# Optimization experiments

Hardware: AMD Instinct MI355X
Metric: run time of the kernel (lower is better)

Reference implementation:

```python
import jax, jax.numpy as jnp
import numpy as np

N_NODES = 100000
N_EDGES = 800000
IN_CH = 64
NUM_CLASSES = 64


def setup_inputs() -> dict:
    key = jax.random.key(0)
    k_x, k_e, k_w, k_b, k_fw, k_fb = jax.random.split(key, 6)
    x = jax.random.normal(k_x, (N_NODES, IN_CH), dtype=jnp.float32)
    edge_index = jax.random.randint(k_e, (2, N_EDGES), 0, N_NODES, dtype=jnp.int64)
    # GCNConv(in_channels, in_channels): weight + bias
    s = 1.0 / np.sqrt(IN_CH)
    W = jax.random.uniform(k_w, (IN_CH, IN_CH), jnp.float32, -s, s)
    b = jax.random.uniform(k_b, (IN_CH,), jnp.float32, -s, s)
    # LayerNorm(in_channels)
    gamma = jnp.ones((IN_CH,), jnp.float32)
    beta = jnp.zeros((IN_CH,), jnp.float32)
    # fc: Linear(in_channels, num_classes)
    fcW = jax.random.uniform(k_fw, (IN_CH, NUM_CLASSES), jnp.float32, -s, s)
    fcb = jax.random.uniform(k_fb, (NUM_CLASSES,), jnp.float32, -s, s)
    return {"x": x, "edge_index": edge_index, "W": W, "b": b,
            "gamma": gamma, "beta": beta, "fcW": fcW, "fcb": fcb}


def _gcn_conv(x, src, dst, W, b, n_nodes):
    # PyG GCNConv: linear transform, add self-loops, sym-normalized scatter-add.
    loop = jnp.arange(n_nodes, dtype=src.dtype)
    src = jnp.concatenate([src, loop])
    dst = jnp.concatenate([dst, loop])
    deg = jax.ops.segment_sum(jnp.ones(dst.shape, x.dtype), dst, num_segments=n_nodes)
    dinv = jax.lax.rsqrt(deg)  # deg >= 1 thanks to self-loops
    norm = dinv[src] * dinv[dst]  # [E+N]
    h = x @ W  # [N, C]
    msg = h[src] * norm[:, None]  # [E+N, C]
    out = jax.ops.segment_sum(msg, dst, num_segments=n_nodes)
    return out + b


def _layer_norm(x, gamma, beta, eps=1e-5):
    mu = jnp.mean(x, axis=-1, keepdims=True)
    var = jnp.mean(jnp.square(x - mu), axis=-1, keepdims=True)
    return (x - mu) * jax.lax.rsqrt(var + eps) * gamma + beta


def reference(x, edge_index, W, b, gamma, beta, fcW, fcb):
    n_nodes = x.shape[0]
    src, dst = edge_index[0], edge_index[1]
    h = _gcn_conv(x, src, dst, W, b, n_nodes)
    h = _layer_norm(h, gamma, beta)
    h = jax.nn.relu(h)
    # dropout is identity in eval mode
    h = h * x  # dot-product gating with original input
    return h @ fcW + fcb
```

## Files before the change

### kernel.cpp

```cpp
#include <hip/hip_runtime.h>
#include <hip/hip_fp16.h>
#include <math.h>

#define N_NODES 100000
#define N_EDGES 800000
#define C 64
#define SLOT 48
#define XW_BLOCKS 391
#define EDGE_BLOCKS 3125

#define XCOMP(v, c) ((c) == 0 ? (v).x : (c) == 1 ? (v).y : (c) == 2 ? (v).z : (v).w)

__device__ inline unsigned pk2h(float a, float b) {
    __half2 h = __floats2half2_rn(a, b);
    return *(unsigned*)&h;
}

__global__ __launch_bounds__(256) void fill_xw_kernel(
        const int* __restrict__ src, const int* __restrict__ dst,
        int* __restrict__ cnt, int* __restrict__ srcs,
        const float* __restrict__ x, const float* __restrict__ W,
        uint4* __restrict__ hs4) {
    if (blockIdx.x >= XW_BLOCKS) {
        const int e = (blockIdx.x - XW_BLOCKS) * 256 + threadIdx.x;
        const int d = dst[e];
        const int p = atomicAdd(&cnt[d], 1);
        if (p < SLOT) srcs[d * SLOT + p] = src[e];
        return;
    }
    const int lane = threadIdx.x & 63;
    const int wv = blockIdx.x * 4 + (threadIdx.x >> 6);
    const int r = wv * 64 + lane;
    const bool valid = r < N_NODES;
    const float4* __restrict__ x4 = (const float4*)x;

    float acc[C];
#pragma unroll
    for (int m = 0; m < C; ++m) acc[m] = 0.0f;

    for (int kk = 0; kk < 4; ++kk) {
        float4 xv[4];
#pragma unroll
        for (int q = 0; q < 4; ++q)
            xv[q] = valid ? x4[r * 16 + kk * 4 + q] : make_float4(0.f, 0.f, 0.f, 0.f);
#pragma unroll
        for (int j = 0; j < 16; ++j) {
            const float xs = XCOMP(xv[j >> 2], j & 3);
            const float* __restrict__ wr = W + (kk * 16 + j) * C;
#pragma unroll
            for (int m = 0; m < C; ++m) acc[m] = fmaf(xs, wr[m], acc[m]);
        }
    }

    if (valid) {
#pragma unroll
        for (int q = 0; q < 8; ++q) {
            uint4 u;
            u.x = pk2h(acc[8 * q + 0], acc[8 * q + 1]);
            u.y = pk2h(acc[8 * q + 2], acc[8 * q + 3]);
            u.z = pk2h(acc[8 * q + 4], acc[8 * q + 5]);
            u.w = pk2h(acc[8 * q + 6], acc[8 * q + 7]);
            hs4[r * 8 + q] = u;
        }
    }
}

__global__ __launch_bounds__(256) void gather_ln_kernel(
        const uint4* __restrict__ hs4, const int* __restrict__ cnt,
        const int* __restrict__ srcs, const float4* __restrict__ x4,
        const float* __restrict__ b, const float* __restrict__ gamma,
        const float* __restrict__ beta, float4* __restrict__ g4) {
    const int lane = threadIdx.x & 63;
    const int n = blockIdx.x * 4 + (threadIdx.x >> 6);
    const int eg = lane >> 3;
    const int cg = lane & 7;

    const int deg = cnt[n];
    const int dg = deg < SLOT ? deg : SLOT;
    const int base = n * SLOT;
    const float dinv = rsqrtf((float)deg + 1.0f);

    float a[8];
    if (eg == 0) {
        const uint4 hv = hs4[n * 8 + cg];
        const float2 f0 = __half22float2(*(const __half2*)&hv.x);
        const float2 f1 = __half22float2(*(const __half2*)&hv.y);
        const float2 f2 = __half22float2(*(const __half2*)&hv.z);
        const float2 f3 = __half22float2(*(const __half2*)&hv.w);
        a[0] = dinv * f0.x; a[1] = dinv * f0.y; a[2] = dinv * f1.x; a[3] = dinv * f1.y;
        a[4] = dinv * f2.x; a[5] = dinv * f2.y; a[6] = dinv * f3.x; a[7] = dinv * f3.y;
    } else {
#pragma unroll
        for (int i = 0; i < 8; ++i) a[i] = 0.0f;
    }

    for (int j = eg; j < dg; j += 8) {
        const int s = srcs[base + j];
        const float ds = rsqrtf((float)cnt[s] + 1.0f);
        const uint4 hv = hs4[s * 8 + cg];
        const float2 f0 = __half22float2(*(const __half2*)&hv.x);
        const float2 f1 = __half22float2(*(const __half2*)&hv.y);
        const float2 f2 = __half22float2(*(const __half2*)&hv.z);
        const float2 f3 = __half22float2(*(const __half2*)&hv.w);
        a[0] = fmaf(ds, f0.x, a[0]); a[1] = fmaf(ds, f0.y, a[1]);
        a[2] = fmaf(ds, f1.x, a[2]); a[3] = fmaf(ds, f1.y, a[3]);
        a[4] = fmaf(ds, f2.x, a[4]); a[5] = fmaf(ds, f2.y, a[5]);
        a[6] = fmaf(ds, f3.x, a[6]); a[7] = fmaf(ds, f3.y, a[7]);
    }

#pragma unroll
    for (int o = 8; o <= 32; o <<= 1) {
#pragma unroll
        for (int i = 0; i < 8; ++i) a[i] += __shfl_xor(a[i], o);
    }

    const float4* __restrict__ b4 = (const float4*)b;
    const float4 b0 = b4[cg * 2], b1 = b4[cg * 2 + 1];

    float t[8];
    t[0] = dinv * a[0] + b0.x; t[1] = dinv * a[1] + b0.y;
    t[2] = dinv * a[2] + b0.z; t[3] = dinv * a[3] + b0.w;
    t[4] = dinv * a[4] + b1.x; t[5] = dinv * a[5] + b1.y;
    t[6] = dinv * a[6] + b1.z; t[7] = dinv * a[7] + b1.w;

    float s1 = t[0] + t[1] + t[2] + t[3] + t[4] + t[5] + t[6] + t[7];
#pragma unroll
    for (int o = 1; o <= 4; o <<= 1) s1 += __shfl_xor(s1, o);
    const float mu = s1 * (1.0f / 64.0f);

    float d[8], s2 = 0.f;
#pragma unroll
    for (int i = 0; i < 8; ++i) { d[i] = t[i] - mu; s2 = fmaf(d[i], d[i], s2); }
#pragma unroll
    for (int o = 1; o <= 4; o <<= 1) s2 += __shfl_xor(s2, o);
    const float rstd = rsqrtf(s2 * (1.0f / 64.0f) + 1e-5f);

    const float4* __restrict__ gm4 = (const float4*)gamma;
    const float4* __restrict__ bt4 = (const float4*)beta;
    const float4 gm0 = gm4[cg * 2], gm1 = gm4[cg * 2 + 1];
    const float4 bt0 = bt4[cg * 2], bt1 = bt4[cg * 2 + 1];
    const float4 xv0 = x4[n * 16 + cg * 2], xv1 = x4[n * 16 + cg * 2 + 1];

    if (eg == 0) {
        float4 o0, o1;
        o0.x = fmaxf(d[0] * rstd * gm0.x + bt0.x, 0.f) * xv0.x;
        o0.y = fmaxf(d[1] * rstd * gm0.y + bt0.y, 0.f) * xv0.y;
        o0.z = fmaxf(d[2] * rstd * gm0.z + bt0.z, 0.f) * xv0.z;
        o0.w = fmaxf(d[3] * rstd * gm0.w + bt0.w, 0.f) * xv0.w;
        o1.x = fmaxf(d[4] * rstd * gm1.x + bt1.x, 0.f) * xv1.x;
        o1.y = fmaxf(d[5] * rstd * gm1.y + bt1.y, 0.f) * xv1.y;
        o1.z = fmaxf(d[6] * rstd * gm1.z + bt1.z, 0.f) * xv1.z;
        o1.w = fmaxf(d[7] * rstd * gm1.w + bt1.w, 0.f) * xv1.w;
        g4[n * 16 + cg * 2]     = o0;
        g4[n * 16 + cg * 2 + 1] = o1;
    }
}

__global__ __launch_bounds__(256) void fc_kernel(const float* g,
                                                 const float* __restrict__ fcW,
                                                 const float* __restrict__ fcb,
                                                 float* out) {
    const int lane = threadIdx.x & 63;
    const int wv = blockIdx.x * 4 + (threadIdx.x >> 6);
    const int r = wv * 64 + lane;
    const bool valid = r < N_NODES;
    const float4* g4 = (const float4*)g;

    float acc[C];
#pragma unroll
    for (int m = 0; m < C; ++m) acc[m] = fcb[m];

    for (int kk = 0; kk < 4; ++kk) {
        float4 gv[4];
#pragma unroll
        for (int q = 0; q < 4; ++q)
            gv[q] = valid ? g4[r * 16 + kk * 4 + q] : make_float4(0.f, 0.f, 0.f, 0.f);
#pragma unroll
        for (int j = 0; j < 16; ++j) {
            const float gs = XCOMP(gv[j >> 2], j & 3);
            const float* __restrict__ wr = fcW + (kk * 16 + j) * C;
#pragma unroll
            for (int m = 0; m < C; ++m) acc[m] = fmaf(gs, wr[m], acc[m]);
        }
    }

    if (valid) {
        float4* out4 = (float4*)out;
#pragma unroll
        for (int q = 0; q < 16; ++q)
            out4[r * 16 + q] = make_float4(acc[4 * q], acc[4 * q + 1],
                                           acc[4 * q + 2], acc[4 * q + 3]);
    }
}

extern "C" void kernel_launch(void* const* d_in, const int* in_sizes, int n_in,
                              void* d_out, int out_size, void* d_ws, size_t ws_size,
                              hipStream_t stream) {
    const float* x     = (const float*)d_in[0];
    const int*   ei    = (const int*)d_in[1];
    const float* W     = (const float*)d_in[2];
    const float* b     = (const float*)d_in[3];
    const float* gamma = (const float*)d_in[4];
    const float* beta  = (const float*)d_in[5];
    const float* fcW   = (const float*)d_in[6];
    const float* fcb   = (const float*)d_in[7];
    float* out = (float*)d_out;

    const int* srcI = ei;
    const int* dstI = ei + N_EDGES;

    int*  cnt  = (int*)d_ws;
    int*  srcs = cnt + 100352;
    uint4* hs4 = (uint4*)(srcs + N_NODES * SLOT);

    float* g = out;

    hipMemsetAsync(cnt, 0, N_NODES * sizeof(int), stream);

    fill_xw_kernel<<<XW_BLOCKS + EDGE_BLOCKS, 256, 0, stream>>>(srcI, dstI, cnt, srcs,
                                                                x, W, hs4);

    gather_ln_kernel<<<N_NODES / 4, 256, 0, stream>>>(hs4, cnt, srcs, (const float4*)x,
                                                      b, gamma, beta, (float4*)g);

    fc_kernel<<<XW_BLOCKS, 256, 0, stream>>>(g, fcW, fcb, out);
}
```

Measured before the change: 240.9 us.

## Bucket edges by destination block then bin in shared memory

```diff
diff --git a/kernel.cpp b/kernel.cpp
--- a/kernel.cpp
+++ b/kernel.cpp
@@ -6,6 +6,8 @@
 #define N_EDGES 800000
 #define C 64
 #define SLOT 48
+#define NB 391
+#define CAP 2560
 #define XW_BLOCKS 391
 #define EDGE_BLOCKS 3125
 
@@ -16,16 +18,19 @@
     return *(unsigned*)&h;
 }
 
-__global__ __launch_bounds__(256) void fill_xw_kernel(
+__global__ __launch_bounds__(256) void xw_bucket_kernel(
         const int* __restrict__ src, const int* __restrict__ dst,
-        int* __restrict__ cnt, int* __restrict__ srcs,
+        int* __restrict__ cur, unsigned* __restrict__ bdata,
         const float* __restrict__ x, const float* __restrict__ W,
         uint4* __restrict__ hs4) {
     if (blockIdx.x >= XW_BLOCKS) {
         const int e = (blockIdx.x - XW_BLOCKS) * 256 + threadIdx.x;
         const int d = dst[e];
-        const int p = atomicAdd(&cnt[d], 1);
-        if (p < SLOT) srcs[d * SLOT + p] = src[e];
+        const int s = src[e];
+        const int bkt = d >> 8;
+        const int p = atomicAdd(&cur[bkt * 16], 1);
+        if (p < CAP)
+            bdata[bkt * CAP + p] = ((unsigned)(d & 255) << 17) | (unsigned)s;
         return;
     }
     const int lane = threadIdx.x & 63;
@@ -65,11 +70,45 @@
     }
 }
 
+__global__ __launch_bounds__(256) void bin_kernel(
+        const int* __restrict__ cur, const unsigned* __restrict__ bdata,
+        int* __restrict__ srcs, int* __restrict__ cnt, float* __restrict__ dinv) {
+    __shared__ int fcnt[256];
+    __shared__ int bins[256 * SLOT];
+    const int b = blockIdx.x;
+    const int tid = threadIdx.x;
+    const int n0 = b << 8;
+    const int nvalid = (N_NODES - n0) < 256 ? (N_NODES - n0) : 256;
+
+    fcnt[tid] = 0;
+    __syncthreads();
+
+    const int cb = cur[b * 16] < CAP ? cur[b * 16] : CAP;
+    for (int i = tid; i < cb; i += 256) {
+        const unsigned w = bdata[b * CAP + i];
+        const int id = (int)(w >> 17);
+        const int s = (int)(w & 0x1FFFF);
+        const int p = atomicAdd(&fcnt[id], 1);
+        if (p < SLOT) bins[id * SLOT + p] = s;
+    }
+    __syncthreads();
+
+    if (tid < nvalid) {
+        const int c = fcnt[tid];
+        cnt[n0 + tid] = c;
+        dinv[n0 + tid] = rsqrtf((float)c + 1.0f);
+    }
+    const int tot = nvalid * SLOT;
+    for (int i = tid; i < tot; i += 256)
+        srcs[n0 * SLOT + i] = bins[i];
+}
+
 __global__ __launch_bounds__(256) void gather_ln_kernel(
         const uint4* __restrict__ hs4, const int* __restrict__ cnt,
-        const int* __restrict__ srcs, const float4* __restrict__ x4,
-        const float* __restrict__ b, const float* __restrict__ gamma,
-        const float* __restrict__ beta, float4* __restrict__ g4) {
+        const float* __restrict__ dinvA, const int* __restrict__ srcs,
+        const float4* __restrict__ x4, const float* __restrict__ b,
+        const float* __restrict__ gamma, const float* __restrict__ beta,
+        float4* __restrict__ g4) {
     const int lane = threadIdx.x & 63;
     const int n = blockIdx.x * 4 + (threadIdx.x >> 6);
     const int eg = lane >> 3;
@@ -78,7 +117,7 @@
     const int deg = cnt[n];
     const int dg = deg < SLOT ? deg : SLOT;
     const int base = n * SLOT;
-    const float dinv = rsqrtf((float)deg + 1.0f);
+    const float dinv = dinvA[n];
 
     float a[8];
     if (eg == 0) {
@@ -96,7 +135,7 @@
 
     for (int j = eg; j < dg; j += 8) {
         const int s = srcs[base + j];
-        const float ds = rsqrtf((float)cnt[s] + 1.0f);
+        const float ds = dinvA[s];
         const uint4 hv = hs4[s * 8 + cg];
         const float2 f0 = __half22float2(*(const __half2*)&hv.x);
         const float2 f1 = __half22float2(*(const __half2*)&hv.y);
@@ -209,19 +248,25 @@
     const int* srcI = ei;
     const int* dstI = ei + N_EDGES;
 
-    int*  cnt  = (int*)d_ws;
-    int*  srcs = cnt + 100352;
-    uint4* hs4 = (uint4*)(srcs + N_NODES * SLOT);
+    int*      cur   = (int*)d_ws;
+    unsigned* bdata = (unsigned*)(cur + 8192);
+    int*      srcs  = (int*)(bdata + NB * CAP);
+    int*      cnt   = srcs + N_NODES * SLOT;
+    float*    dinv  = (float*)(cnt + 100352);
+    uint4*    hs4   = (uint4*)(dinv + 100352);
 
     float* g = out;
 
-    hipMemsetAsync(cnt, 0, N_NODES * sizeof(int), stream);
-
-    fill_xw_kernel<<<XW_BLOCKS + EDGE_BLOCKS, 256, 0, stream>>>(srcI, dstI, cnt, srcs,
-                                                                x, W, hs4);
-
-    gather_ln_kernel<<<N_NODES / 4, 256, 0, stream>>>(hs4, cnt, srcs, (const float4*)x,
-                                                      b, gamma, beta, (float4*)g);
+    hipMemsetAsync(cur, 0, NB * 16 * sizeof(int), stream);
+
+    xw_bucket_kernel<<<XW_BLOCKS + EDGE_BLOCKS, 256, 0, stream>>>(srcI, dstI, cur,
+                                                                  bdata, x, W, hs4);
+
+    bin_kernel<<<NB, 256, 0, stream>>>(cur, bdata, srcs, cnt, dinv);
+
+    gather_ln_kernel<<<N_NODES / 4, 256, 0, stream>>>(hs4, cnt, dinv, srcs,
+                                                      (const float4*)x, b, gamma,
+                                                      beta, (float4*)g);
 
     fc_kernel<<<XW_BLOCKS, 256, 0, stream>>>(g, fcW, fcb, out);
 }
```

New measurement: 242.1 us. About the same (+0.5%).
